# Kernel optimization log

Measured on AMD Instinct MI355X. Metric: run time of the kernel, lower is better.

The kernel has to match this reference:

```python
import jax, jax.numpy as jnp
import numpy as np

SPATIAL_SHAPES = [(58, 100)]  # single level (H, W)
N_HEADS, N_LEVELS, N_POINTS, NUM_CAMS = 8, 1, 8, 6
D_MODEL = 256


def _bilinear_sample(v, loc, h, w):
    # v: (B, h, w, H, d); loc: (B, Lq, H, P, 2) normalized to [0,1]
    # matches F.grid_sample(mode='bilinear', padding_mode='zeros', align_corners=False)
    x = loc[..., 0] * w - 0.5
    y = loc[..., 1] * h - 0.5
    x0 = jnp.floor(x)
    y0 = jnp.floor(y)
    fx = x - x0
    fy = y - y0
    x0i = x0.astype(jnp.int32)
    y0i = y0.astype(jnp.int32)
    B, Hh = v.shape[0], v.shape[3]
    b = jnp.arange(B)[:, None, None, None]
    hd = jnp.arange(Hh)[None, None, :, None]

    def g(yi, xi):
        valid = ((yi >= 0) & (yi < h) & (xi >= 0) & (xi < w)).astype(v.dtype)
        yc = jnp.clip(yi, 0, h - 1)
        xc = jnp.clip(xi, 0, w - 1)
        return v[b, yc, xc, hd] * valid[..., None]  # (B,Lq,H,P,d)

    return (g(y0i, x0i) * ((1 - fy) * (1 - fx))[..., None]
            + g(y0i, x0i + 1) * ((1 - fy) * fx)[..., None]
            + g(y0i + 1, x0i) * (fy * (1 - fx))[..., None]
            + g(y0i + 1, x0i + 1) * (fy * fx)[..., None])


def _ms_deform_attn(value, locs, weights):
    # value: (B, S, H, d); locs: (B,Lq,H,L,P,2); weights: (B,Lq,H,L,P)
    B, S, Hh, d = value.shape
    out = 0.0
    start = 0
    for l, (h, w) in enumerate(SPATIAL_SHAPES):
        v = value[:, start:start + h * w].reshape(B, h, w, Hh, d)
        start += h * w
        samp = _bilinear_sample(v, locs[:, :, :, l], h, w)  # (B,Lq,H,P,d)
        out = out + jnp.einsum('bqhpd,bqhp->bqhd', samp, weights[:, :, :, l])
    return out.reshape(B, -1, Hh * d)


def setup_inputs() -> dict:
    key = jax.random.key(0)
    ks = jax.random.split(key, 12)
    B, Lq, C = 1, 22500, D_MODEL
    S = sum(h * w for h, w in SPATIAL_SHAPES)
    inp = {
        'query': jax.random.normal(ks[0], (B, Lq, C), jnp.float32),
        'reference_points_cam': jax.random.uniform(ks[1], (NUM_CAMS, B, Lq, 4, 2), jnp.float32),
        'bev_mask': jax.random.randint(ks[2], (NUM_CAMS, B, Lq, 4), 0, 2, jnp.int32),
        'value': jax.random.normal(ks[3], (B * NUM_CAMS, S, C), jnp.float32),
        'W_off': jax.random.normal(ks[4], (N_HEADS * N_LEVELS * N_POINTS * 2, C), jnp.float32) * 0.01,
        'b_off': jax.random.normal(ks[5], (N_HEADS * N_LEVELS * N_POINTS * 2,), jnp.float32),
        'W_attn': jax.random.normal(ks[6], (N_HEADS * N_LEVELS * N_POINTS, C), jnp.float32) * 0.02,
        'b_attn': jnp.zeros((N_HEADS * N_LEVELS * N_POINTS,), jnp.float32),
        'W_val': jax.random.normal(ks[7], (C, C), jnp.float32) * (1.0 / np.sqrt(C)),
        'b_val': jnp.zeros((C,), jnp.float32),
        'W_out': jax.random.normal(ks[8], (C, C), jnp.float32) * (1.0 / np.sqrt(C)),
        'b_out': jnp.zeros((C,), jnp.float32),
    }
    return inp


def reference(query, reference_points_cam, bev_mask, value,
              W_off, b_off, W_attn, b_attn, W_val, b_val, W_out, b_out):
    B, Lq, C = query.shape
    d = C // N_HEADS
    D = reference_points_cam.shape[3]  # num_Z_anchors = 4
    S = value.shape[1]

    # value_proj for all cameras; value rows are laid out as b*num_cams + cam
    val = value @ W_val.T + b_val
    val = val.reshape(B, NUM_CAMS, S, N_HEADS, d).transpose(1, 0, 2, 3, 4)  # (cams,B,S,H,d)

    # query-side projections are camera-independent
    off = (query @ W_off.T + b_off).reshape(B, Lq, N_HEADS, N_LEVELS, N_POINTS, 2)
    normalizer = jnp.array([[w, h] for (h, w) in SPATIAL_SHAPES], dtype=query.dtype)  # (L,2)
    off = off / normalizer[None, None, None, :, None, :]
    off = off.reshape(B, Lq, N_HEADS, N_LEVELS, N_POINTS // D, D, 2)

    aw = (query @ W_attn.T + b_attn).reshape(B, Lq, N_HEADS, N_LEVELS * N_POINTS)
    aw = jax.nn.softmax(aw, axis=-1).reshape(B, Lq, N_HEADS, N_LEVELS, N_POINTS)

    vis = (bev_mask.sum(-1) > 0)  # (cams, B, Lq)
    slots = jnp.zeros_like(query)
    for cam in range(NUM_CAMS):  # small fixed camera set
        ref = reference_points_cam[cam][:, :, None, None, None, :, :]  # (B,Lq,1,1,1,D,2)
        locs = (ref + off).reshape(B, Lq, N_HEADS, N_LEVELS, N_POINTS, 2)
        out = _ms_deform_attn(val[cam], locs, aw)  # (B,Lq,C)
        slots = slots + out * vis[cam][..., None].astype(query.dtype)

    count = jnp.maximum(vis.sum(0).astype(query.dtype), 1.0)  # (B,Lq)
    slots = slots / count[..., None]
    return slots @ W_out.T + b_out
```

## Files before the change

### kernel.cpp

```cpp
#include <hip/hip_runtime.h>

#define LQ     22500
#define SPA_H  58
#define SPA_W  100
#define S_TOT  5800
#define NCAMS  6
#define CDIM   256

typedef __attribute__((ext_vector_type(8))) _Float16 half8;
typedef __attribute__((ext_vector_type(4))) _Float16 half4;
typedef __attribute__((ext_vector_type(2))) _Float16 half2v;
typedef __attribute__((ext_vector_type(4))) float f32x4;

__device__ __forceinline__ half8 cvt8(f32x4 lo, f32x4 hi) {
  half8 r;
  r[0] = (_Float16)lo.x; r[1] = (_Float16)lo.y; r[2] = (_Float16)lo.z; r[3] = (_Float16)lo.w;
  r[4] = (_Float16)hi.x; r[5] = (_Float16)hi.y; r[6] = (_Float16)hi.z; r[7] = (_Float16)hi.w;
  return r;
}

__global__ __launch_bounds__(256) void cvt_w(
    const float* __restrict__ W_val, const float* __restrict__ W_off,
    const float* __restrict__ W_attn, const float* __restrict__ W_out,
    _Float16* __restrict__ Wv, _Float16* __restrict__ Wcat,
    _Float16* __restrict__ Wo) {
  const int e = (blockIdx.x * 256 + threadIdx.x) * 4;
  const float* src; _Float16* dst; int off;
  if (e < 65536)       { src = W_val;  dst = Wv;   off = e; }
  else if (e < 98304)  { src = W_off;  dst = Wcat; off = e - 65536; }
  else if (e < 114688) { src = W_attn; dst = Wcat + 32768; off = e - 98304; }
  else if (e < 180224) { src = W_out;  dst = Wo;   off = e - 114688; }
  else return;
  f32x4 v = *(const f32x4*)(src + off);
  half4 o;
  o[0] = (_Float16)v.x; o[1] = (_Float16)v.y; o[2] = (_Float16)v.z; o[3] = (_Float16)v.w;
  *(half4*)(dst + off) = o;
}

template<int N>
__device__ __forceinline__ void gemm_body_af32(
    const float* __restrict__ A, const _Float16* __restrict__ W,
    const float* __restrict__ bias, const float* __restrict__ bias2,
    _Float16* __restrict__ C, int M, int rowbase) {
  constexpr int NT = N / 64;
  const int lane = threadIdx.x & 63;
  const int wave = threadIdx.x >> 6;
  const int m15  = lane & 15;
  const int quad = lane >> 4;
  const int colbase = wave * (N / 4);
  const int kq = quad * 8;

  const float* ap[4];
#pragma unroll
  for (int rt = 0; rt < 4; ++rt) {
    int r = rowbase + rt * 16 + m15;
    r = r < M ? r : M - 1;
    ap[rt] = A + (size_t)r * 256 + kq;
  }
  const _Float16* wp[NT];
#pragma unroll
  for (int t = 0; t < NT; ++t)
    wp[t] = W + (size_t)(colbase + t * 16 + m15) * 256 + kq;

  f32x4 acc[4][NT];
#pragma unroll
  for (int rt = 0; rt < 4; ++rt)
#pragma unroll
    for (int t = 0; t < NT; ++t) acc[rt][t] = (f32x4){0.f, 0.f, 0.f, 0.f};

  f32x4 al0[4], ah0[4], al1[4], ah1[4];
  half8 b0[NT], b1[NT];

#define LOADSET(AL, AH, BB, KO) \
  { _Pragma("unroll") for (int rt = 0; rt < 4; ++rt) { \
      AL[rt] = *(const f32x4*)(ap[rt] + (KO)); \
      AH[rt] = *(const f32x4*)(ap[rt] + (KO) + 4); } \
    _Pragma("unroll") for (int t = 0; t < NT; ++t) \
      BB[t] = *(const half8*)(wp[t] + (KO)); }
#define MFMASET(AL, AH, BB) \
  { half8 af[4]; \
    _Pragma("unroll") for (int rt = 0; rt < 4; ++rt) af[rt] = cvt8(AL[rt], AH[rt]); \
    _Pragma("unroll") for (int t = 0; t < NT; ++t) \
      _Pragma("unroll") for (int rt = 0; rt < 4; ++rt) \
        acc[rt][t] = __builtin_amdgcn_mfma_f32_16x16x32_f16(af[rt], BB[t], acc[rt][t], 0, 0, 0); }

  LOADSET(al0, ah0, b0, 0)
#pragma unroll 1
  for (int kk = 0; kk < 192; kk += 64) {
    LOADSET(al1, ah1, b1, kk + 32)
    MFMASET(al0, ah0, b0)
    LOADSET(al0, ah0, b0, kk + 64)
    MFMASET(al1, ah1, b1)
  }
  LOADSET(al1, ah1, b1, 224)
  MFMASET(al0, ah0, b0)
  MFMASET(al1, ah1, b1)
#undef LOADSET
#undef MFMASET

#pragma unroll
  for (int rt = 0; rt < 4; ++rt) {
    const int orow = rowbase + rt * 16 + quad * 4;
#pragma unroll
    for (int t = 0; t < NT; ++t) {
      const int col = colbase + t * 16 + m15;
      const float bv = (N == 192 && col >= 128) ? bias2[col - 128] : bias[col];
#pragma unroll
      for (int i = 0; i < 4; ++i) {
        const int r = orow + i;
        if (r < M) C[(size_t)r * 256 + col] = (_Float16)(acc[rt][t][i] + bv);
      }
    }
  }
}

__global__ __launch_bounds__(256, 2) void gemm_inputs(
    const float* __restrict__ value, const float* __restrict__ query,
    const _Float16* __restrict__ Wv, const _Float16* __restrict__ Wcat,
    const float* __restrict__ b_val, const float* __restrict__ b_off,
    const float* __restrict__ b_attn,
    _Float16* __restrict__ vp, _Float16* __restrict__ qproj) {
  const int b = blockIdx.x;
  if (b < 544) gemm_body_af32<256>(value, Wv, b_val, b_val, vp, 34800, b * 64);
  else         gemm_body_af32<192>(query, Wcat, b_off, b_attn, qproj, LQ, (b - 544) * 64);
}

__global__ __launch_bounds__(256) void sampler_fused(
    const _Float16* __restrict__ vp,
    const _Float16* __restrict__ qproj,
    const float* __restrict__ ref,
    const int* __restrict__ bev,
    const _Float16* __restrict__ Wo,
    const float* __restrict__ b_out,
    float* __restrict__ out)
{
  const int t  = threadIdx.x;
  const int ql = t >> 5;
  const int s  = t & 31;
  const int h  = s >> 2;
  const int q0 = blockIdx.x * 8;
  const int q  = q0 + ql;
  const bool qok = q < LQ;

  __shared__ float s_off[8][8][17];
  __shared__ float s_w8[8][8][9];
  __shared__ float s_ref[8][48];
  __shared__ float s_vis[8][6];
  __shared__ _Float16 s_slots[16][264];

  {
    half8 z = {};
    _Float16* sl = &s_slots[0][0];
#pragma unroll
    for (int rep = 0; rep < 3; ++rep) {
      const int idx = t + rep * 256;
      if (idx < 528) *(half8*)(sl + idx * 8) = z;
    }
  }

  if (qok) {
    if (s < 24) {
      half8 qc = *(const half8*)(qproj + (size_t)q * 256 + s * 8);
      if (s < 16) {
#pragma unroll
        for (int i = 0; i < 8; ++i) {
          const int f = s * 8 + i;
          s_off[ql][f >> 4][f & 15] =
              (float)qc[i] * ((f & 1) ? (1.f / 58.f) : (1.f / 100.f));
        }
      } else {
        const int hh = s - 16;
        float m = -1e30f;
#pragma unroll
        for (int p = 0; p < 8; ++p) m = fmaxf(m, (float)qc[p]);
        float e[8], ssum = 0.f;
#pragma unroll
        for (int p = 0; p < 8; ++p) { e[p] = __expf((float)qc[p] - m); ssum += e[p]; }
        const float inv = 1.f / ssum;
#pragma unroll
        for (int p = 0; p < 8; ++p) s_w8[ql][hh][p] = e[p] * inv;
      }
    }
    if (s < 12) {
      const int cam = s >> 1, half = s & 1;
      f32x4 r = *(const f32x4*)(ref + ((size_t)cam * LQ + q) * 8 + half * 4);
      *(f32x4*)&s_ref[ql][s * 4] = r;
    }
    if (s < 6) {
      int4 bm = *(const int4*)(bev + ((size_t)s * LQ + q) * 4);
      s_vis[ql][s] = (bm.x + bm.y + bm.z + bm.w) > 0 ? 1.f : 0.f;
    }
  }
  __syncthreads();

  float acc[8];
#pragma unroll
  for (int i = 0; i < 8; ++i) acc[i] = 0.f;

  if (qok) {
    float cnt = 0.f;
#pragma unroll
    for (int c = 0; c < 6; ++c) cnt += s_vis[ql][c];
    const float invc = 1.f / fmaxf(cnt, 1.f);

#pragma unroll 1
    for (int cam = 0; cam < NCAMS; ++cam) {
      const float visf = s_vis[ql][cam];
      const _Float16* vpc = vp + (size_t)cam * (S_TOT * CDIM) + s * 8;
#pragma unroll 2
      for (int p = 0; p < 8; ++p) {
        const int z = p & 3;
        const float x = (s_ref[ql][cam * 8 + z * 2 + 0] + s_off[ql][h][p * 2 + 0]) * 100.f - 0.5f;
        const float y = (s_ref[ql][cam * 8 + z * 2 + 1] + s_off[ql][h][p * 2 + 1]) * 58.f - 0.5f;
        const float x0f = floorf(x), y0f = floorf(y);
        const float fx = x - x0f, fy = y - y0f;
        const int x0 = (int)x0f, y0 = (int)y0f;
        const float vx0 = (x0 >= 0 && x0 < SPA_W) ? 1.f : 0.f;
        const float vx1 = (x0 >= -1 && x0 < SPA_W - 1) ? 1.f : 0.f;
        const float vy0 = (y0 >= 0 && y0 < SPA_H) ? 1.f : 0.f;
        const float vy1 = (y0 >= -1 && y0 < SPA_H - 1) ? 1.f : 0.f;
        const int xc0 = min(max(x0, 0), SPA_W - 1), xc1 = min(max(x0 + 1, 0), SPA_W - 1);
        const int yc0 = min(max(y0, 0), SPA_H - 1), yc1 = min(max(y0 + 1, 0), SPA_H - 1);
        const float wgt = s_w8[ql][h][p] * visf;
        const float wy0 = (1.f - fy) * vy0 * wgt, wy1 = fy * vy1 * wgt;
        const float bx0 = (1.f - fx) * vx0,       bx1 = fx * vx1;
        const float w00 = wy0 * bx0, w01 = wy0 * bx1;
        const float w10 = wy1 * bx0, w11 = wy1 * bx1;
        half8 v00 = *(const half8*)(vpc + (size_t)(yc0 * SPA_W + xc0) * CDIM);
        half8 v01 = *(const half8*)(vpc + (size_t)(yc0 * SPA_W + xc1) * CDIM);
        half8 v10 = *(const half8*)(vpc + (size_t)(yc1 * SPA_W + xc0) * CDIM);
        half8 v11 = *(const half8*)(vpc + (size_t)(yc1 * SPA_W + xc1) * CDIM);
#if __has_builtin(__builtin_amdgcn_fdot2)
        half2v wa; wa[0] = (_Float16)w00; wa[1] = (_Float16)w01;
        half2v wb; wb[0] = (_Float16)w10; wb[1] = (_Float16)w11;
#pragma unroll
        for (int i = 0; i < 8; ++i) {
          half2v va; va[0] = v00[i]; va[1] = v01[i];
          half2v vb; vb[0] = v10[i]; vb[1] = v11[i];
          acc[i] = __builtin_amdgcn_fdot2(va, wa, acc[i], false);
          acc[i] = __builtin_amdgcn_fdot2(vb, wb, acc[i], false);
        }
#else
#pragma unroll
        for (int i = 0; i < 8; ++i) {
          acc[i] = fmaf(w00, (float)v00[i], acc[i]);
          acc[i] = fmaf(w01, (float)v01[i], acc[i]);
          acc[i] = fmaf(w10, (float)v10[i], acc[i]);
          acc[i] = fmaf(w11, (float)v11[i], acc[i]);
        }
#endif
      }
    }

    half8 o;
#pragma unroll
    for (int i = 0; i < 8; ++i) o[i] = (_Float16)(acc[i] * invc);
    *(half8*)(&s_slots[ql][s * 8]) = o;
  }
  __syncthreads();

  const int lane = t & 63;
  const int wave = t >> 6;
  const int m15  = lane & 15;
  const int quad = lane >> 4;
  const int colbase = wave * 64;

  f32x4 acc4[4];
#pragma unroll
  for (int tt = 0; tt < 4; ++tt) acc4[tt] = (f32x4){0.f, 0.f, 0.f, 0.f};

  const _Float16* arow = &s_slots[m15][quad * 8];
  const _Float16* wp[4];
#pragma unroll
  for (int tt = 0; tt < 4; ++tt)
    wp[tt] = Wo + (size_t)(colbase + tt * 16 + m15) * 256 + quad * 8;

#pragma unroll 2
  for (int kk = 0; kk < 256; kk += 32) {
    half8 a = *(const half8*)(arow + kk);
#pragma unroll
    for (int tt = 0; tt < 4; ++tt) {
      half8 b = *(const half8*)(wp[tt] + kk);
      acc4[tt] = __builtin_amdgcn_mfma_f32_16x16x32_f16(a, b, acc4[tt], 0, 0, 0);
    }
  }

#pragma unroll
  for (int tt = 0; tt < 4; ++tt) {
    const int col = colbase + tt * 16 + m15;
    const float bv = b_out[col];
#pragma unroll
    for (int i = 0; i < 4; ++i) {
      const int row = quad * 4 + i;
      if (row < 8 && q0 + row < LQ)
        out[(size_t)(q0 + row) * 256 + col] = acc4[tt][i] + bv;
    }
  }
}

extern "C" void kernel_launch(void* const* d_in, const int* in_sizes, int n_in,
                              void* d_out, int out_size, void* d_ws, size_t ws_size,
                              hipStream_t stream) {
  const float* query  = (const float*)d_in[0];
  const float* refpts = (const float*)d_in[1];
  const int*   bev    = (const int*)d_in[2];
  const float* value  = (const float*)d_in[3];
  const float* W_off  = (const float*)d_in[4];
  const float* b_off  = (const float*)d_in[5];
  const float* W_attn = (const float*)d_in[6];
  const float* b_attn = (const float*)d_in[7];
  const float* W_val  = (const float*)d_in[8];
  const float* b_val  = (const float*)d_in[9];
  const float* W_out  = (const float*)d_in[10];
  const float* b_out  = (const float*)d_in[11];

  char* ws = (char*)d_ws;
  _Float16* vp    = (_Float16*)(ws + 0);
  _Float16* qproj = (_Float16*)(ws + 17817600);
  _Float16* Wv    = (_Float16*)(ws + 29337600);
  _Float16* Wcat  = (_Float16*)(ws + 29468672);
  _Float16* Wo    = (_Float16*)(ws + 29566976);

  cvt_w<<<176, 256, 0, stream>>>(W_val, W_off, W_attn, W_out, Wv, Wcat, Wo);

  gemm_inputs<<<896, 256, 0, stream>>>(value, query, Wv, Wcat,
                                       b_val, b_off, b_attn, vp, qproj);

  sampler_fused<<<(LQ + 7) / 8, 256, 0, stream>>>(vp, qproj, refpts, bev,
                                                  Wo, b_out, (float*)d_out);
}
```

Baseline: 450.5 us.

## Split output projection into separate GEMM kernel and skip invisible cameras

Moves the output projection out of the sampler into its own 32-row MFMA GEMM kernel. Sampled slots are written in fp16 into the qproj buffer, which each query's block has already finished reading. The sampler now runs 4 queries per 128-thread block with no slot tile in shared memory, and skips cameras where the query is not visible. The input GEMMs are also retiled from 64 to 32 rows per block. This removes the half-empty 16-row MFMA tiles and the extra LDS from the fused epilogue, at the cost of an extra kernel launch and a global round trip for the slots.

Result: slower. 491.0 us (+9.0%).

```diff
diff --git a/kernel.cpp b/kernel.cpp
--- a/kernel.cpp
+++ b/kernel.cpp
@@ -50,9 +50,9 @@
   const int colbase = wave * (N / 4);
   const int kq = quad * 8;
 
-  const float* ap[4];
-#pragma unroll
-  for (int rt = 0; rt < 4; ++rt) {
+  const float* ap[2];
+#pragma unroll
+  for (int rt = 0; rt < 2; ++rt) {
     int r = rowbase + rt * 16 + m15;
     r = r < M ? r : M - 1;
     ap[rt] = A + (size_t)r * 256 + kq;
@@ -62,26 +62,26 @@
   for (int t = 0; t < NT; ++t)
     wp[t] = W + (size_t)(colbase + t * 16 + m15) * 256 + kq;
 
-  f32x4 acc[4][NT];
-#pragma unroll
-  for (int rt = 0; rt < 4; ++rt)
+  f32x4 acc[2][NT];
+#pragma unroll
+  for (int rt = 0; rt < 2; ++rt)
 #pragma unroll
     for (int t = 0; t < NT; ++t) acc[rt][t] = (f32x4){0.f, 0.f, 0.f, 0.f};
 
-  f32x4 al0[4], ah0[4], al1[4], ah1[4];
+  f32x4 al0[2], ah0[2], al1[2], ah1[2];
   half8 b0[NT], b1[NT];
 
 #define LOADSET(AL, AH, BB, KO) \
-  { _Pragma("unroll") for (int rt = 0; rt < 4; ++rt) { \
+  { _Pragma("unroll") for (int rt = 0; rt < 2; ++rt) { \
       AL[rt] = *(const f32x4*)(ap[rt] + (KO)); \
       AH[rt] = *(const f32x4*)(ap[rt] + (KO) + 4); } \
     _Pragma("unroll") for (int t = 0; t < NT; ++t) \
       BB[t] = *(const half8*)(wp[t] + (KO)); }
 #define MFMASET(AL, AH, BB) \
-  { half8 af[4]; \
-    _Pragma("unroll") for (int rt = 0; rt < 4; ++rt) af[rt] = cvt8(AL[rt], AH[rt]); \
+  { half8 af[2]; \
+    _Pragma("unroll") for (int rt = 0; rt < 2; ++rt) af[rt] = cvt8(AL[rt], AH[rt]); \
     _Pragma("unroll") for (int t = 0; t < NT; ++t) \
-      _Pragma("unroll") for (int rt = 0; rt < 4; ++rt) \
+      _Pragma("unroll") for (int rt = 0; rt < 2; ++rt) \
         acc[rt][t] = __builtin_amdgcn_mfma_f32_16x16x32_f16(af[rt], BB[t], acc[rt][t], 0, 0, 0); }
 
   LOADSET(al0, ah0, b0, 0)
@@ -99,7 +99,7 @@
 #undef MFMASET
 
 #pragma unroll
-  for (int rt = 0; rt < 4; ++rt) {
+  for (int rt = 0; rt < 2; ++rt) {
     const int orow = rowbase + rt * 16 + quad * 4;
 #pragma unroll
     for (int t = 0; t < NT; ++t) {
@@ -114,49 +114,104 @@
   }
 }
 
-__global__ __launch_bounds__(256, 2) void gemm_inputs(
+__global__ __launch_bounds__(256) void gemm_inputs(
     const float* __restrict__ value, const float* __restrict__ query,
     const _Float16* __restrict__ Wv, const _Float16* __restrict__ Wcat,
     const float* __restrict__ b_val, const float* __restrict__ b_off,
     const float* __restrict__ b_attn,
     _Float16* __restrict__ vp, _Float16* __restrict__ qproj) {
   const int b = blockIdx.x;
-  if (b < 544) gemm_body_af32<256>(value, Wv, b_val, b_val, vp, 34800, b * 64);
-  else         gemm_body_af32<192>(query, Wcat, b_off, b_attn, qproj, LQ, (b - 544) * 64);
-}
-
-__global__ __launch_bounds__(256) void sampler_fused(
+  if (b < 1088) gemm_body_af32<256>(value, Wv, b_val, b_val, vp, 34800, b * 32);
+  else          gemm_body_af32<192>(query, Wcat, b_off, b_attn, qproj, LQ, (b - 1088) * 32);
+}
+
+__global__ __launch_bounds__(256) void gemm_out_k(
+    const _Float16* __restrict__ A, const _Float16* __restrict__ W,
+    const float* __restrict__ bias, float* __restrict__ out) {
+  constexpr int NT = 4;
+  const int lane = threadIdx.x & 63;
+  const int wave = threadIdx.x >> 6;
+  const int m15  = lane & 15;
+  const int quad = lane >> 4;
+  const int rowbase = blockIdx.x * 32;
+  const int colbase = wave * 64;
+  const int kq = quad * 8;
+
+  const _Float16* ap[2];
+#pragma unroll
+  for (int rt = 0; rt < 2; ++rt) {
+    int r = rowbase + rt * 16 + m15;
+    r = r < LQ ? r : LQ - 1;
+    ap[rt] = A + (size_t)r * 256 + kq;
+  }
+  const _Float16* wp[NT];
+#pragma unroll
+  for (int t = 0; t < NT; ++t)
+    wp[t] = W + (size_t)(colbase + t * 16 + m15) * 256 + kq;
+
+  f32x4 acc[2][NT];
+#pragma unroll
+  for (int rt = 0; rt < 2; ++rt)
+#pragma unroll
+    for (int t = 0; t < NT; ++t) acc[rt][t] = (f32x4){0.f, 0.f, 0.f, 0.f};
+
+  half8 a0[2], b0[NT], a1[2], b1[NT];
+#define LOADSET(AA, BB, KO) \
+  { _Pragma("unroll") for (int rt = 0; rt < 2; ++rt) AA[rt] = *(const half8*)(ap[rt] + (KO)); \
+    _Pragma("unroll") for (int t = 0; t < NT; ++t)  BB[t]  = *(const half8*)(wp[t] + (KO)); }
+#define MFMASET(AA, BB) \
+  { _Pragma("unroll") for (int t = 0; t < NT; ++t) \
+      _Pragma("unroll") for (int rt = 0; rt < 2; ++rt) \
+        acc[rt][t] = __builtin_amdgcn_mfma_f32_16x16x32_f16(AA[rt], BB[t], acc[rt][t], 0, 0, 0); }
+
+  LOADSET(a0, b0, 0)
+#pragma unroll 1
+  for (int kk = 0; kk < 192; kk += 64) {
+    LOADSET(a1, b1, kk + 32)
+    MFMASET(a0, b0)
+    LOADSET(a0, b0, kk + 64)
+    MFMASET(a1, b1)
+  }
+  LOADSET(a1, b1, 224)
+  MFMASET(a0, b0)
+  MFMASET(a1, b1)
+#undef LOADSET
+#undef MFMASET
+
+#pragma unroll
+  for (int rt = 0; rt < 2; ++rt) {
+    const int orow = rowbase + rt * 16 + quad * 4;
+#pragma unroll
+    for (int t = 0; t < NT; ++t) {
+      const int col = colbase + t * 16 + m15;
+      const float bv = bias[col];
+#pragma unroll
+      for (int i = 0; i < 4; ++i) {
+        const int r = orow + i;
+        if (r < LQ) out[(size_t)r * 256 + col] = acc[rt][t][i] + bv;
+      }
+    }
+  }
+}
+
+__global__ __launch_bounds__(128) void sampler(
     const _Float16* __restrict__ vp,
     const _Float16* __restrict__ qproj,
     const float* __restrict__ ref,
     const int* __restrict__ bev,
-    const _Float16* __restrict__ Wo,
-    const float* __restrict__ b_out,
-    float* __restrict__ out)
+    _Float16* __restrict__ slots)
 {
   const int t  = threadIdx.x;
   const int ql = t >> 5;
   const int s  = t & 31;
   const int h  = s >> 2;
-  const int q0 = blockIdx.x * 8;
-  const int q  = q0 + ql;
+  const int q  = blockIdx.x * 4 + ql;
   const bool qok = q < LQ;
 
-  __shared__ float s_off[8][8][17];
-  __shared__ float s_w8[8][8][9];
-  __shared__ float s_ref[8][48];
-  __shared__ float s_vis[8][6];
-  __shared__ _Float16 s_slots[16][264];
-
-  {
-    half8 z = {};
-    _Float16* sl = &s_slots[0][0];
-#pragma unroll
-    for (int rep = 0; rep < 3; ++rep) {
-      const int idx = t + rep * 256;
-      if (idx < 528) *(half8*)(sl + idx * 8) = z;
-    }
-  }
+  __shared__ float s_off[4][8][17];
+  __shared__ float s_w8[4][8][9];
+  __shared__ float s_ref[4][48];
+  __shared__ float s_vis[4][6];
 
   if (qok) {
     if (s < 24) {
@@ -182,8 +237,8 @@
       }
     }
     if (s < 12) {
-      const int cam = s >> 1, half = s & 1;
-      f32x4 r = *(const f32x4*)(ref + ((size_t)cam * LQ + q) * 8 + half * 4);
+      const int cam = s >> 1, hf = s & 1;
+      f32x4 r = *(const f32x4*)(ref + ((size_t)cam * LQ + q) * 8 + hf * 4);
       *(f32x4*)&s_ref[ql][s * 4] = r;
     }
     if (s < 6) {
@@ -192,110 +247,70 @@
     }
   }
   __syncthreads();
+  if (!qok) return;
+
+  float cnt = 0.f;
+#pragma unroll
+  for (int c = 0; c < 6; ++c) cnt += s_vis[ql][c];
+  const float invc = 1.f / fmaxf(cnt, 1.f);
 
   float acc[8];
 #pragma unroll
   for (int i = 0; i < 8; ++i) acc[i] = 0.f;
 
-  if (qok) {
-    float cnt = 0.f;
-#pragma unroll
-    for (int c = 0; c < 6; ++c) cnt += s_vis[ql][c];
-    const float invc = 1.f / fmaxf(cnt, 1.f);
-
 #pragma unroll 1
-    for (int cam = 0; cam < NCAMS; ++cam) {
-      const float visf = s_vis[ql][cam];
-      const _Float16* vpc = vp + (size_t)cam * (S_TOT * CDIM) + s * 8;
+  for (int cam = 0; cam < NCAMS; ++cam) {
+    if (s_vis[ql][cam] == 0.f) continue;
+    const _Float16* vpc = vp + (size_t)cam * (S_TOT * CDIM) + s * 8;
 #pragma unroll 2
-      for (int p = 0; p < 8; ++p) {
-        const int z = p & 3;
-        const float x = (s_ref[ql][cam * 8 + z * 2 + 0] + s_off[ql][h][p * 2 + 0]) * 100.f - 0.5f;
-        const float y = (s_ref[ql][cam * 8 + z * 2 + 1] + s_off[ql][h][p * 2 + 1]) * 58.f - 0.5f;
-        const float x0f = floorf(x), y0f = floorf(y);
-        const float fx = x - x0f, fy = y - y0f;
-        const int x0 = (int)x0f, y0 = (int)y0f;
-        const float vx0 = (x0 >= 0 && x0 < SPA_W) ? 1.f : 0.f;
-        const float vx1 = (x0 >= -1 && x0 < SPA_W - 1) ? 1.f : 0.f;
-        const float vy0 = (y0 >= 0 && y0 < SPA_H) ? 1.f : 0.f;
-        const float vy1 = (y0 >= -1 && y0 < SPA_H - 1) ? 1.f : 0.f;
-        const int xc0 = min(max(x0, 0), SPA_W - 1), xc1 = min(max(x0 + 1, 0), SPA_W - 1);
-        const int yc0 = min(max(y0, 0), SPA_H - 1), yc1 = min(max(y0 + 1, 0), SPA_H - 1);
-        const float wgt = s_w8[ql][h][p] * visf;
-        const float wy0 = (1.f - fy) * vy0 * wgt, wy1 = fy * vy1 * wgt;
-        const float bx0 = (1.f - fx) * vx0,       bx1 = fx * vx1;
-        const float w00 = wy0 * bx0, w01 = wy0 * bx1;
-        const float w10 = wy1 * bx0, w11 = wy1 * bx1;
-        half8 v00 = *(const half8*)(vpc + (size_t)(yc0 * SPA_W + xc0) * CDIM);
-        half8 v01 = *(const half8*)(vpc + (size_t)(yc0 * SPA_W + xc1) * CDIM);
-        half8 v10 = *(const half8*)(vpc + (size_t)(yc1 * SPA_W + xc0) * CDIM);
-        half8 v11 = *(const half8*)(vpc + (size_t)(yc1 * SPA_W + xc1) * CDIM);
+    for (int p = 0; p < 8; ++p) {
+      const int z = p & 3;
+      const float x = (s_ref[ql][cam * 8 + z * 2 + 0] + s_off[ql][h][p * 2 + 0]) * 100.f - 0.5f;
+      const float y = (s_ref[ql][cam * 8 + z * 2 + 1] + s_off[ql][h][p * 2 + 1]) * 58.f - 0.5f;
+      const float x0f = floorf(x), y0f = floorf(y);
+      const float fx = x - x0f, fy = y - y0f;
+      const int x0 = (int)x0f, y0 = (int)y0f;
+      const float vx0 = (x0 >= 0 && x0 < SPA_W) ? 1.f : 0.f;
+      const float vx1 = (x0 >= -1 && x0 < SPA_W - 1) ? 1.f : 0.f;
+      const float vy0 = (y0 >= 0 && y0 < SPA_H) ? 1.f : 0.f;
+      const float vy1 = (y0 >= -1 && y0 < SPA_H - 1) ? 1.f : 0.f;
+      const int xc0 = min(max(x0, 0), SPA_W - 1), xc1 = min(max(x0 + 1, 0), SPA_W - 1);
+      const int yc0 = min(max(y0, 0), SPA_H - 1), yc1 = min(max(y0 + 1, 0), SPA_H - 1);
+      const float wgt = s_w8[ql][h][p];
+      const float wy0 = (1.f - fy) * vy0 * wgt, wy1 = fy * vy1 * wgt;
+      const float bx0 = (1.f - fx) * vx0,       bx1 = fx * vx1;
+      const float w00 = wy0 * bx0, w01 = wy0 * bx1;
+      const float w10 = wy1 * bx0, w11 = wy1 * bx1;
+      half8 v00 = *(const half8*)(vpc + (size_t)(yc0 * SPA_W + xc0) * CDIM);
+      half8 v01 = *(const half8*)(vpc + (size_t)(yc0 * SPA_W + xc1) * CDIM);
+      half8 v10 = *(const half8*)(vpc + (size_t)(yc1 * SPA_W + xc0) * CDIM);
+      half8 v11 = *(const half8*)(vpc + (size_t)(yc1 * SPA_W + xc1) * CDIM);
 #if __has_builtin(__builtin_amdgcn_fdot2)
-        half2v wa; wa[0] = (_Float16)w00; wa[1] = (_Float16)w01;
-        half2v wb; wb[0] = (_Float16)w10; wb[1] = (_Float16)w11;
-#pragma unroll
-        for (int i = 0; i < 8; ++i) {
-          half2v va; va[0] = v00[i]; va[1] = v01[i];
-          half2v vb; vb[0] = v10[i]; vb[1] = v11[i];
-          acc[i] = __builtin_amdgcn_fdot2(va, wa, acc[i], false);
-          acc[i] = __builtin_amdgcn_fdot2(vb, wb, acc[i], false);
-        }
+      half2v wa; wa[0] = (_Float16)w00; wa[1] = (_Float16)w01;
+      half2v wb; wb[0] = (_Float16)w10; wb[1] = (_Float16)w11;
+#pragma unroll
+      for (int i = 0; i < 8; ++i) {
+        half2v va; va[0] = v00[i]; va[1] = v01[i];
+        half2v vb; vb[0] = v10[i]; vb[1] = v11[i];
+        acc[i] = __builtin_amdgcn_fdot2(va, wa, acc[i], false);
+        acc[i] = __builtin_amdgcn_fdot2(vb, wb, acc[i], false);
+      }
 #else
 #pragma unroll
-        for (int i = 0; i < 8; ++i) {
-          acc[i] = fmaf(w00, (float)v00[i], acc[i]);
-          acc[i] = fmaf(w01, (float)v01[i], acc[i]);
-          acc[i] = fmaf(w10, (float)v10[i], acc[i]);
-          acc[i] = fmaf(w11, (float)v11[i], acc[i]);
-        }
+      for (int i = 0; i < 8; ++i) {
+        acc[i] = fmaf(w00, (float)v00[i], acc[i]);
+        acc[i] = fmaf(w01, (float)v01[i], acc[i]);
+        acc[i] = fmaf(w10, (float)v10[i], acc[i]);
+        acc[i] = fmaf(w11, (float)v11[i], acc[i]);
+      }
 #endif
-      }
-    }
-
-    half8 o;
-#pragma unroll
-    for (int i = 0; i < 8; ++i) o[i] = (_Float16)(acc[i] * invc);
-    *(half8*)(&s_slots[ql][s * 8]) = o;
-  }
-  __syncthreads();
-
-  const int lane = t & 63;
-  const int wave = t >> 6;
-  const int m15  = lane & 15;
-  const int quad = lane >> 4;
-  const int colbase = wave * 64;
-
-  f32x4 acc4[4];
-#pragma unroll
-  for (int tt = 0; tt < 4; ++tt) acc4[tt] = (f32x4){0.f, 0.f, 0.f, 0.f};
-
-  const _Float16* arow = &s_slots[m15][quad * 8];
-  const _Float16* wp[4];
-#pragma unroll
-  for (int tt = 0; tt < 4; ++tt)
-    wp[tt] = Wo + (size_t)(colbase + tt * 16 + m15) * 256 + quad * 8;
-
-#pragma unroll 2
-  for (int kk = 0; kk < 256; kk += 32) {
-    half8 a = *(const half8*)(arow + kk);
-#pragma unroll
-    for (int tt = 0; tt < 4; ++tt) {
-      half8 b = *(const half8*)(wp[tt] + kk);
-      acc4[tt] = __builtin_amdgcn_mfma_f32_16x16x32_f16(a, b, acc4[tt], 0, 0, 0);
-    }
-  }
-
-#pragma unroll
-  for (int tt = 0; tt < 4; ++tt) {
-    const int col = colbase + tt * 16 + m15;
-    const float bv = b_out[col];
-#pragma unroll
-    for (int i = 0; i < 4; ++i) {
-      const int row = quad * 4 + i;
-      if (row < 8 && q0 + row < LQ)
-        out[(size_t)(q0 + row) * 256 + col] = acc4[tt][i] + bv;
-    }
-  }
+    }
+  }
+
+  half8 o;
+#pragma unroll
+  for (int i = 0; i < 8; ++i) o[i] = (_Float16)(acc[i] * invc);
+  *(half8*)(slots + (size_t)q * 256 + s * 8) = o;
 }
 
 extern "C" void kernel_launch(void* const* d_in, const int* in_sizes, int n_in,
@@ -323,9 +338,10 @@
 
   cvt_w<<<176, 256, 0, stream>>>(W_val, W_off, W_attn, W_out, Wv, Wcat, Wo);
 
-  gemm_inputs<<<896, 256, 0, stream>>>(value, query, Wv, Wcat,
-                                       b_val, b_off, b_attn, vp, qproj);
-
-  sampler_fused<<<(LQ + 7) / 8, 256, 0, stream>>>(vp, qproj, refpts, bev,
-                                                  Wo, b_out, (float*)d_out);
-}
+  gemm_inputs<<<1792, 256, 0, stream>>>(value, query, Wv, Wcat,
+                                        b_val, b_off, b_attn, vp, qproj);
+
+  sampler<<<(LQ + 3) / 4, 128, 0, stream>>>(vp, qproj, refpts, bev, qproj);
+
+  gemm_out_k<<<(LQ + 31) / 32, 256, 0, stream>>>(qproj, Wo, b_out, (float*)d_out);
+}
```
